# Performance work log

Measured on AMD Instinct MI355X. Metric: run time of the kernel, lower is better.

## Reference

```python
import jax, jax.numpy as jnp
import numpy as np
import math

D_MODEL = 256
N_LEVELS = 4
N_HEADS = 8
N_POINTS = 4
N_FRAME = 4
SHAPES = [(80, 80), (40, 40), (20, 20), (10, 10)]  # sum H*W = 8500
NB = 2
T1 = 4
T2 = 4
LEN_Q = 8500


def _grid_init_bias():
    # replicate torch _reset_parameters grid bias for sampling_offsets
    thetas = np.arange(N_HEADS, dtype=np.float32) * (2.0 * math.pi / N_HEADS)
    grid = np.stack([np.cos(thetas), np.sin(thetas)], -1)
    grid = grid / np.abs(grid).max(-1, keepdims=True)
    grid = np.tile(grid[:, None, None, :], (1, N_LEVELS, N_POINTS, 1))
    grid = grid * (np.arange(N_POINTS, dtype=np.float32) + 1.0)[None, None, :, None]
    return jnp.asarray(grid.reshape(-1), jnp.float32)


def setup_inputs() -> dict:
    key = jax.random.key(0)
    ks = jax.random.split(key, 8)
    Len_in = sum(h * w for h, w in SHAPES)
    query = jax.random.normal(ks[0], (NB, T1, LEN_Q, D_MODEL), jnp.float32)
    reference_points = jax.random.uniform(ks[1], (NB, T1, LEN_Q, N_LEVELS, 2), jnp.float32)
    input_flatten = jax.random.normal(ks[2], (NB, T2, Len_in, D_MODEL), jnp.float32)
    input_spatial_shapes = jnp.array(SHAPES, jnp.int32)
    starts = np.cumsum([0] + [h * w for h, w in SHAPES])[:-1]
    input_level_start_index = jnp.asarray(starts, jnp.int32)
    s = 0.01
    W_off = jax.random.normal(ks[3], (D_MODEL, N_HEADS * N_LEVELS * N_POINTS * 2), jnp.float32) * s
    b_off = _grid_init_bias()
    W_att = jax.random.normal(ks[4], (D_MODEL, N_HEADS * N_LEVELS * N_POINTS), jnp.float32) * s
    b_att = jnp.zeros((N_HEADS * N_LEVELS * N_POINTS,), jnp.float32)
    xav = 1.0 / math.sqrt(D_MODEL)
    W_val = jax.random.normal(ks[5], (D_MODEL, D_MODEL), jnp.float32) * xav
    b_val = jnp.zeros((D_MODEL,), jnp.float32)
    W_out = jax.random.normal(ks[6], (D_MODEL, D_MODEL), jnp.float32) * xav
    b_out = jnp.zeros((D_MODEL,), jnp.float32)
    return dict(query=query, reference_points=reference_points, input_flatten=input_flatten,
                input_spatial_shapes=input_spatial_shapes, input_level_start_index=input_level_start_index,
                W_off=W_off, b_off=b_off, W_att=W_att, b_att=b_att,
                W_val=W_val, b_val=b_val, W_out=W_out, b_out=b_out)


def _bilinear(v_flat, H, W, gx, gy):
    # v_flat: (B, d, H*W); gx,gy: (B, S) in [-1,1]; zeros padding, align_corners=False
    x = (gx + 1.0) * (W * 0.5) - 0.5
    y = (gy + 1.0) * (H * 0.5) - 0.5
    x0 = jnp.floor(x); y0 = jnp.floor(y)
    x1 = x0 + 1.0; y1 = y0 + 1.0
    wx1 = x - x0; wx0 = 1.0 - wx1
    wy1 = y - y0; wy0 = 1.0 - wy1

    def gather(xi, yi):
        valid = ((xi >= 0) & (xi < W) & (yi >= 0) & (yi < H)).astype(v_flat.dtype)
        xc = jnp.clip(xi, 0, W - 1).astype(jnp.int32)
        yc = jnp.clip(yi, 0, H - 1).astype(jnp.int32)
        idx = yc * W + xc  # (B, S)
        g = jnp.take_along_axis(v_flat, idx[:, None, :], axis=2)  # (B, d, S)
        return g * valid[:, None, :]

    return (gather(x0, y0) * (wx0 * wy0)[:, None, :]
            + gather(x1, y0) * (wx1 * wy0)[:, None, :]
            + gather(x0, y1) * (wx0 * wy1)[:, None, :]
            + gather(x1, y1) * (wx1 * wy1)[:, None, :])


def _core(value_t, locs, att, shapes):
    # value_t: (n, Len_in, M, d); locs: (n, Lq, M, L, P, 2); att: (n, Lq, M, L, P)
    n, Len_in, M, d = value_t.shape
    Lq, P = locs.shape[1], locs.shape[4]
    start = 0
    out = 0.0
    for l, (H, W) in enumerate(shapes):
        hw = H * W
        v = value_t[:, start:start + hw]  # (n, hw, M, d)
        start += hw
        v = v.transpose(0, 2, 3, 1).reshape(n * M, d, hw)
        g = locs[:, :, :, l] * 2.0 - 1.0  # (n, Lq, M, P, 2)
        g = g.transpose(0, 2, 1, 3, 4).reshape(n * M, Lq * P, 2)
        samp = _bilinear(v, H, W, g[..., 0], g[..., 1])  # (n*M, d, Lq*P)
        a = att[:, :, :, l].transpose(0, 2, 1, 3).reshape(n * M, 1, Lq * P)
        out = out + (samp * a).reshape(n, M, d, Lq, P).sum(-1)
    return out.transpose(0, 3, 1, 2).reshape(n, Lq, M * d)  # (n, Lq, C)


def reference(query, reference_points, input_flatten, input_spatial_shapes, input_level_start_index,
              W_off, b_off, W_att, b_att, W_val, b_val, W_out, b_out):
    shapes = [(int(h), int(w)) for h, w in np.asarray(input_spatial_shapes)]
    n, t1n, Lq, C = query.shape
    M, L, P = N_HEADS, N_LEVELS, N_POINTS
    d = C // M
    value = input_flatten @ W_val + b_val  # (n, T2, Len_in, C)
    value = value.reshape(n, value.shape[1], -1, M, d)
    normalizer = jnp.array([[w, h] for h, w in shapes], jnp.float32)  # (L, 2) = (W_l, H_l)
    outs = []
    for t1 in range(t1n):
        t2s = [t for t in (t1 - 1, t1, t1 + 1) if 0 <= t < N_FRAME]
        K = len(t2s)
        q = query[:, t1]  # (n, Lq, C)
        # all frames share ONE attention_weights Linear -> identical logits per t2
        logits = (q @ W_att + b_att).reshape(n, Lq, M, L, P)
        stacked = jnp.broadcast_to(logits[..., None], (n, Lq, M, L, P, K))
        att = jax.nn.softmax(stacked.reshape(n, Lq, M, L * P * K), axis=-1)
        att = att.reshape(n, Lq, M, L, P, K)
        # all frames share ONE sampling_offsets Linear -> identical locations per t2
        off = (q @ W_off + b_off).reshape(n, Lq, M, L, P, 2)
        off = off / normalizer[None, None, None, :, None, :]
        locs = reference_points[:, t1][:, :, None, :, None, :] + off  # (n,Lq,M,L,P,2)
        out_t1 = 0.0
        for k, t2 in enumerate(t2s):
            out_t1 = out_t1 + _core(value[:, t2], locs, att[..., k], shapes)
        outs.append(out_t1)
    out = jnp.stack(outs, axis=1)  # (n, T1, Lq, C)
    return out @ W_out + b_out
```

## Files before the change

kernel.cpp:

```cpp
#include <hip/hip_runtime.h>

#define LQ 8500

typedef _Float16 half8 __attribute__((ext_vector_type(8)));
typedef _Float16 h2 __attribute__((ext_vector_type(2)));
typedef float f32x4 __attribute__((ext_vector_type(4)));

__device__ __forceinline__ unsigned short f2h(float f) {
    return __builtin_bit_cast(unsigned short, (_Float16)f);
}
__device__ __forceinline__ float hlo(unsigned w) {
    return (float)__builtin_bit_cast(_Float16, (unsigned short)(w & 0xffffu));
}
__device__ __forceinline__ float hhi(unsigned w) {
    return (float)__builtin_bit_cast(_Float16, (unsigned short)(w >> 16));
}
__device__ __forceinline__ unsigned pk2(float a, float b) {
    return (unsigned)f2h(a) | ((unsigned)f2h(b) << 16);
}
__device__ __forceinline__ h2 toh2(unsigned w) { return __builtin_bit_cast(h2, w); }

__global__ __launch_bounds__(256) void prep_weights(const float* __restrict__ Woff,
                                                    const float* __restrict__ boff,
                                                    const float* __restrict__ Watt,
                                                    const float* __restrict__ batt,
                                                    const float* __restrict__ Wval,
                                                    const float* __restrict__ Wout,
                                                    unsigned short* __restrict__ Wct,
                                                    unsigned short* __restrict__ Wvt,
                                                    unsigned short* __restrict__ Wot,
                                                    float* __restrict__ bcat) {
    int idx = blockIdx.x * 256 + threadIdx.x;
    if (idx < 98304) {
        int j = idx >> 8, k = idx & 255;
        float v = (j < 256) ? Woff[k * 256 + j] : Watt[k * 128 + (j - 256)];
        Wct[idx] = f2h(v);
    } else if (idx < 98304 + 65536) {
        int t = idx - 98304;
        int n = t >> 8, k = t & 255;
        Wvt[t] = f2h(Wval[k * 256 + n]);
    } else if (idx < 98304 + 131072) {
        int t = idx - 98304 - 65536;
        int n = t >> 8, k = t & 255;
        Wot[t] = f2h(Wout[k * 256 + n]);
    } else if (idx < 98304 + 131072 + 384) {
        int j = idx - 98304 - 131072;
        bcat[j] = (j < 256) ? boff[j] : batt[j - 256];
    }
}

__global__ __launch_bounds__(256) void sum_frames(const float4* __restrict__ inp,
                                                  uint4* __restrict__ Xs) {
    int g = blockIdx.y;
    int t1 = g & 3, n = g >> 2;
    int f = blockIdx.x * 256 + threadIdx.x;
    if (f >= LQ * 32) return;
    int t2a = t1 == 0 ? 0 : t1 - 1;
    int t2b = t1 == 3 ? 3 : t1 + 1;
    float4 s0 = {0, 0, 0, 0}, s1 = {0, 0, 0, 0};
    for (int t2 = t2a; t2 <= t2b; ++t2) {
        const float4* p = inp + (size_t)(n * 4 + t2) * (LQ * 64) + (size_t)f * 2;
        float4 a = p[0], b = p[1];
        s0.x += a.x; s0.y += a.y; s0.z += a.z; s0.w += a.w;
        s1.x += b.x; s1.y += b.y; s1.z += b.z; s1.w += b.w;
    }
    uint4 o;
    o.x = pk2(s0.x, s0.y); o.y = pk2(s0.z, s0.w);
    o.z = pk2(s1.x, s1.y); o.w = pk2(s1.z, s1.w);
    Xs[(size_t)g * (LQ * 32) + f] = o;
}

template <int OUTMODE, int AF32>
__global__ __launch_bounds__(256) void gemm_f16(const void* __restrict__ Avoid,
                                                const unsigned short* __restrict__ Bt,
                                                const float* __restrict__ bias,
                                                void* __restrict__ Cout, int M) {
    __shared__ char lds[16384];
    const int tid = threadIdx.x;
    const int r0 = blockIdx.x * 128, c0 = blockIdx.y * 128;
    const int wid = tid >> 6, lane = tid & 63;
    const int wr = (wid >> 1) * 64, wc = (wid & 1) * 64;

    f32x4 acc[4][4] = {};

    for (int k0 = 0; k0 < 256; k0 += 32) {
#pragma unroll
        for (int cc = 0; cc < 2; ++cc) {
            int ch = cc * 256 + tid;
            int row = ch >> 2, seg = ch & 3;
            int byte = (row << 6) + (seg << 4);
            int swz = byte ^ ((row & 7) << 4);
            uint4 va = {0, 0, 0, 0};
            int ar = r0 + row;
            if (ar < M) {
                if (AF32) {
                    const float4* ap = reinterpret_cast<const float4*>(
                        (const float*)Avoid + (size_t)ar * 256 + k0 + seg * 8);
                    float4 a = ap[0], b = ap[1];
                    va.x = pk2(a.x, a.y); va.y = pk2(a.z, a.w);
                    va.z = pk2(b.x, b.y); va.w = pk2(b.z, b.w);
                } else {
                    va = *reinterpret_cast<const uint4*>(
                        (const unsigned short*)Avoid + (size_t)ar * 256 + k0 + seg * 8);
                }
            }
            *reinterpret_cast<uint4*>(lds + swz) = va;
            uint4 vb = *reinterpret_cast<const uint4*>(Bt + (size_t)(c0 + row) * 256 + k0 + seg * 8);
            *reinterpret_cast<uint4*>(lds + 8192 + swz) = vb;
        }
        __syncthreads();
        half8 af[4], bf[4];
#pragma unroll
        for (int i = 0; i < 4; ++i) {
            int rowA = wr + i * 16 + (lane & 15);
            int byteA = (rowA << 6) + ((lane >> 4) << 4);
            af[i] = *reinterpret_cast<const half8*>(lds + (byteA ^ ((rowA & 7) << 4)));
            int rowB = wc + i * 16 + (lane & 15);
            int byteB = (rowB << 6) + ((lane >> 4) << 4);
            bf[i] = *reinterpret_cast<const half8*>(lds + 8192 + (byteB ^ ((rowB & 7) << 4)));
        }
#pragma unroll
        for (int i = 0; i < 4; ++i)
#pragma unroll
            for (int j = 0; j < 4; ++j)
                acc[i][j] = __builtin_amdgcn_mfma_f32_16x16x32_f16(af[i], bf[j], acc[i][j], 0, 0, 0);
        __syncthreads();
    }

#pragma unroll
    for (int j = 0; j < 4; ++j) {
        int col = c0 + wc + j * 16 + (lane & 15);
        float bv = bias[col];
#pragma unroll
        for (int i = 0; i < 4; ++i) {
#pragma unroll
            for (int r = 0; r < 4; ++r) {
                int row = r0 + wr + i * 16 + (lane >> 4) * 4 + r;
                if (row >= M) continue;
                float v = acc[i][j][r];
                if (OUTMODE == 1) {
                    int g = row / LQ;
                    int pos = row - g * LQ;
                    int t1 = g & 3;
                    float sc = (t1 == 0 || t1 == 3) ? 2.f : 3.f;
                    v += bv * sc;
                    int m = col >> 5, c = col & 31;
                    ((unsigned short*)Cout)[((size_t)(g * 8 + m) * LQ + pos) * 32 + c] = f2h(v);
                } else if (OUTMODE == 2) {
                    ((unsigned short*)Cout)[(size_t)row * 384 + col] = f2h(v + bv);
                } else {
                    ((float*)Cout)[(size_t)row * 256 + col] = v + bv;
                }
            }
        }
    }
}

__global__ __launch_bounds__(256) void sample_kernel(const unsigned short* __restrict__ P,
                                                     const float* __restrict__ refp,
                                                     const unsigned short* __restrict__ Vs,
                                                     unsigned short* __restrict__ O16) {
    int tid = threadIdx.x, bid = blockIdx.x;
    int g = bid & 7;
    int q0 = (bid >> 3) * 16;
    int ql = tid >> 4, m = (tid >> 1) & 7, h = tid & 1;
    int q = q0 + ql;
    if (q >= LQ) return;

    const size_t qrow = (size_t)g * LQ + q;

    unsigned ow[16];
    {
        const uint4* po = reinterpret_cast<const uint4*>(P + qrow * 384 + m * 32);
        uint4 a = po[0], b = po[1], c = po[2], d = po[3];
        ow[0] = a.x; ow[1] = a.y; ow[2] = a.z; ow[3] = a.w;
        ow[4] = b.x; ow[5] = b.y; ow[6] = b.z; ow[7] = b.w;
        ow[8] = c.x; ow[9] = c.y; ow[10] = c.z; ow[11] = c.w;
        ow[12] = d.x; ow[13] = d.y; ow[14] = d.z; ow[15] = d.w;
    }
    float wgt[16];
    {
        const uint4* pa = reinterpret_cast<const uint4*>(P + qrow * 384 + 256 + m * 16);
        uint4 a = pa[0], b = pa[1];
        unsigned aw[8] = {a.x, a.y, a.z, a.w, b.x, b.y, b.z, b.w};
#pragma unroll
        for (int j = 0; j < 8; ++j) {
            wgt[j * 2 + 0] = hlo(aw[j]);
            wgt[j * 2 + 1] = hhi(aw[j]);
        }
        float mx = -1e30f;
#pragma unroll
        for (int j = 0; j < 16; ++j) mx = fmaxf(mx, wgt[j]);
        float s = 0.f;
#pragma unroll
        for (int j = 0; j < 16; ++j) { wgt[j] = __expf(wgt[j] - mx); s += wgt[j]; }
        int t1 = g & 3;
        float Kc = (t1 == 0 || t1 == 3) ? 2.f : 3.f;
        float inv = 1.f / (s * Kc);
#pragma unroll
        for (int j = 0; j < 16; ++j) wgt[j] *= inv;
    }

    float rx[4], ry[4];
    {
        const float4* rp = reinterpret_cast<const float4*>(refp + qrow * 8);
        float4 r0 = rp[0], r1 = rp[1];
        rx[0] = r0.x; ry[0] = r0.y; rx[1] = r0.z; ry[1] = r0.w;
        rx[2] = r1.x; ry[2] = r1.y; rx[3] = r1.z; ry[3] = r1.w;
    }

    h2 acc[8];
#pragma unroll
    for (int d = 0; d < 8; ++d) acc[d] = h2{(_Float16)0.f, (_Float16)0.f};

    const unsigned short* vplane = Vs + (size_t)(g * 8 + m) * (LQ * 32) + h * 16;

#pragma unroll
    for (int p = 0; p < 16; ++p) {
        const int l = p >> 2;
        const int Wl = 80 >> l;
        const int start = (l == 0) ? 0 : (l == 1) ? 6400 : (l == 2) ? 8000 : 8400;
        const float Wlf = (float)Wl;

        float x = fmaf(rx[l], Wlf, hlo(ow[p])) - 0.5f;
        float y = fmaf(ry[l], Wlf, hhi(ow[p])) - 0.5f;
        float w = wgt[p];

        float xf = floorf(x), yf = floorf(y);
        int x0 = (int)xf, y0 = (int)yf;
        float wx1 = x - xf, wy1 = y - yf;

        int xb = min(max(x0, 0), Wl - 2);
        float wl = (x0 == xb) ? 1.f - wx1 : ((x0 + 1 == xb) ? wx1 : 0.f);
        float wr = (x0 == xb) ? wx1 : ((x0 - 1 == xb) ? 1.f - wx1 : 0.f);

        int yc[2];
        float cw[2];
        yc[0] = min(max(y0, 0), Wl - 1);
        cw[0] = (y0 >= 0 && y0 < Wl) ? (1.f - wy1) * w : 0.f;
        int y1i = y0 + 1;
        yc[1] = min(max(y1i, 0), Wl - 1);
        cw[1] = (y1i >= 0 && y1i < Wl) ? wy1 * w : 0.f;

#pragma unroll
        for (int ryi = 0; ryi < 2; ++ryi) {
            float clf = cw[ryi] * wl, crf = cw[ryi] * wr;
            _Float16 clh = (_Float16)clf, crh = (_Float16)crf;
            h2 cl2 = {clh, clh}, cr2 = {crh, crh};
            const uint4* vp = reinterpret_cast<const uint4*>(
                vplane + (size_t)(start + yc[ryi] * Wl + xb) * 32);
            uint4 La = vp[0], Lb = vp[1];
            uint4 Ra = vp[4], Rb = vp[5];
            acc[0] += cl2 * toh2(La.x) + cr2 * toh2(Ra.x);
            acc[1] += cl2 * toh2(La.y) + cr2 * toh2(Ra.y);
            acc[2] += cl2 * toh2(La.z) + cr2 * toh2(Ra.z);
            acc[3] += cl2 * toh2(La.w) + cr2 * toh2(Ra.w);
            acc[4] += cl2 * toh2(Lb.x) + cr2 * toh2(Rb.x);
            acc[5] += cl2 * toh2(Lb.y) + cr2 * toh2(Rb.y);
            acc[6] += cl2 * toh2(Lb.z) + cr2 * toh2(Rb.z);
            acc[7] += cl2 * toh2(Lb.w) + cr2 * toh2(Rb.w);
        }
    }

    unsigned short* op = O16 + qrow * 256 + m * 32 + h * 16;
    uint4 o0, o1;
    o0.x = __builtin_bit_cast(unsigned, acc[0]);
    o0.y = __builtin_bit_cast(unsigned, acc[1]);
    o0.z = __builtin_bit_cast(unsigned, acc[2]);
    o0.w = __builtin_bit_cast(unsigned, acc[3]);
    o1.x = __builtin_bit_cast(unsigned, acc[4]);
    o1.y = __builtin_bit_cast(unsigned, acc[5]);
    o1.z = __builtin_bit_cast(unsigned, acc[6]);
    o1.w = __builtin_bit_cast(unsigned, acc[7]);
    reinterpret_cast<uint4*>(op)[0] = o0;
    reinterpret_cast<uint4*>(op)[1] = o1;
}

extern "C" void kernel_launch(void* const* d_in, const int* in_sizes, int n_in,
                              void* d_out, int out_size, void* d_ws, size_t ws_size,
                              hipStream_t stream) {
    const float* query = (const float*)d_in[0];
    const float* refp  = (const float*)d_in[1];
    const float* inp   = (const float*)d_in[2];
    const float* Woff = (const float*)d_in[5];
    const float* boff = (const float*)d_in[6];
    const float* Watt = (const float*)d_in[7];
    const float* batt = (const float*)d_in[8];
    const float* Wval = (const float*)d_in[9];
    const float* bval = (const float*)d_in[10];
    const float* Wout = (const float*)d_in[11];
    const float* bout = (const float*)d_in[12];
    float* out = (float*)d_out;

    char* base = (char*)d_ws;
    unsigned short* Xs16 = (unsigned short*)base;
    unsigned short* Vs   = (unsigned short*)(base + 34816000);
    unsigned short* P    = (unsigned short*)(base + 69632000);
    unsigned short* Wct  = (unsigned short*)(base + 121856000);
    unsigned short* Wvt  = (unsigned short*)(base + 122052608);
    unsigned short* Wot  = (unsigned short*)(base + 122183680);
    float* bcat          = (float*)(base + 122314752);
    unsigned short* O16  = Xs16;

    prep_weights<<<dim3(898), 256, 0, stream>>>(Woff, boff, Watt, batt, Wval, Wout,
                                                Wct, Wvt, Wot, bcat);

    sum_frames<<<dim3((LQ * 32 + 255) / 256, 8), 256, 0, stream>>>(
        (const float4*)inp, (uint4*)Xs16);

    gemm_f16<1, 0><<<dim3((8 * LQ + 127) / 128, 2), 256, 0, stream>>>(
        Xs16, Wvt, bval, Vs, 8 * LQ);

    gemm_f16<2, 1><<<dim3((8 * LQ + 127) / 128, 3), 256, 0, stream>>>(
        query, Wct, bcat, P, 8 * LQ);

    sample_kernel<<<dim3(((LQ + 15) / 16) * 8), 256, 0, stream>>>(P, refp, Vs, O16);

    gemm_f16<0, 0><<<dim3((8 * LQ + 127) / 128, 2), 256, 0, stream>>>(
        O16, Wot, bout, out, 8 * LQ);
}
```

Before: 363.7 us.

## Fuse frame summation into value GEMM, stage full-K A tile in LDS

Measured after the change: 435.9 us. +19.9%, slower.

```diff
diff --git a/kernel.cpp b/kernel.cpp
--- a/kernel.cpp
+++ b/kernel.cpp
@@ -19,6 +19,10 @@
     return (unsigned)f2h(a) | ((unsigned)f2h(b) << 16);
 }
 __device__ __forceinline__ h2 toh2(unsigned w) { return __builtin_bit_cast(h2, w); }
+__device__ __forceinline__ h2 bc2(float f) {
+    _Float16 h = (_Float16)f;
+    return h2{h, h};
+}
 
 __global__ __launch_bounds__(256) void prep_weights(const float* __restrict__ Woff,
                                                     const float* __restrict__ boff,
@@ -49,82 +53,94 @@
     }
 }
 
-__global__ __launch_bounds__(256) void sum_frames(const float4* __restrict__ inp,
-                                                  uint4* __restrict__ Xs) {
-    int g = blockIdx.y;
-    int t1 = g & 3, n = g >> 2;
-    int f = blockIdx.x * 256 + threadIdx.x;
-    if (f >= LQ * 32) return;
-    int t2a = t1 == 0 ? 0 : t1 - 1;
-    int t2b = t1 == 3 ? 3 : t1 + 1;
-    float4 s0 = {0, 0, 0, 0}, s1 = {0, 0, 0, 0};
-    for (int t2 = t2a; t2 <= t2b; ++t2) {
-        const float4* p = inp + (size_t)(n * 4 + t2) * (LQ * 64) + (size_t)f * 2;
-        float4 a = p[0], b = p[1];
-        s0.x += a.x; s0.y += a.y; s0.z += a.z; s0.w += a.w;
-        s1.x += b.x; s1.y += b.y; s1.z += b.z; s1.w += b.w;
-    }
-    uint4 o;
-    o.x = pk2(s0.x, s0.y); o.y = pk2(s0.z, s0.w);
-    o.z = pk2(s1.x, s1.y); o.w = pk2(s1.z, s1.w);
-    Xs[(size_t)g * (LQ * 32) + f] = o;
-}
-
-template <int OUTMODE, int AF32>
+template <int OUTMODE, int ASRC>
 __global__ __launch_bounds__(256) void gemm_f16(const void* __restrict__ Avoid,
                                                 const unsigned short* __restrict__ Bt,
                                                 const float* __restrict__ bias,
                                                 void* __restrict__ Cout, int M) {
-    __shared__ char lds[16384];
+    __shared__ char lds[65536];
     const int tid = threadIdx.x;
-    const int r0 = blockIdx.x * 128, c0 = blockIdx.y * 128;
+    const int c0 = blockIdx.x * 128, r0 = blockIdx.y * 128;
     const int wid = tid >> 6, lane = tid & 63;
     const int wr = (wid >> 1) * 64, wc = (wid & 1) * 64;
 
+#pragma unroll
+    for (int i = 0; i < 16; ++i) {
+        int c = i * 256 + tid;
+        int t = c >> 9;
+        int row = (c >> 2) & 127;
+        int seg = c & 3;
+        int koff = t * 32 + seg * 8;
+        int ar = r0 + row;
+        uint4 va = {0, 0, 0, 0};
+        if (ar < M) {
+            if (ASRC == 0) {
+                va = *reinterpret_cast<const uint4*>(
+                    (const unsigned short*)Avoid + (size_t)ar * 256 + koff);
+            } else if (ASRC == 1) {
+                const float4* ap = reinterpret_cast<const float4*>(
+                    (const float*)Avoid + (size_t)ar * 256 + koff);
+                float4 a = ap[0], b = ap[1];
+                va.x = pk2(a.x, a.y); va.y = pk2(a.z, a.w);
+                va.z = pk2(b.x, b.y); va.w = pk2(b.z, b.w);
+            } else {
+                int g = ar / LQ;
+                int pos = ar - g * LQ;
+                int t1 = g & 3, n = g >> 2;
+                int tp = t1 == 0 ? 0 : t1 - 1;
+                int tn = t1 == 3 ? 3 : t1 + 1;
+                const float* fb = (const float*)Avoid;
+                const float4* pm = reinterpret_cast<const float4*>(
+                    fb + ((size_t)(n * 4 + t1) * LQ + pos) * 256 + koff);
+                const float4* pp = reinterpret_cast<const float4*>(
+                    fb + ((size_t)(n * 4 + tp) * LQ + pos) * 256 + koff);
+                const float4* pn = reinterpret_cast<const float4*>(
+                    fb + ((size_t)(n * 4 + tn) * LQ + pos) * 256 + koff);
+                float4 m0 = pm[0], m1 = pm[1];
+                float4 a0 = pp[0], a1 = pp[1];
+                float4 b0 = pn[0], b1 = pn[1];
+                float fp = (t1 > 0) ? 1.f : 0.f;
+                float fn = (t1 < 3) ? 1.f : 0.f;
+                float4 s0, s1;
+                s0.x = m0.x + fp * a0.x + fn * b0.x;
+                s0.y = m0.y + fp * a0.y + fn * b0.y;
+                s0.z = m0.z + fp * a0.z + fn * b0.z;
+                s0.w = m0.w + fp * a0.w + fn * b0.w;
+                s1.x = m1.x + fp * a1.x + fn * b1.x;
+                s1.y = m1.y + fp * a1.y + fn * b1.y;
+                s1.z = m1.z + fp * a1.z + fn * b1.z;
+                s1.w = m1.w + fp * a1.w + fn * b1.w;
+                va.x = pk2(s0.x, s0.y); va.y = pk2(s0.z, s0.w);
+                va.z = pk2(s1.x, s1.y); va.w = pk2(s1.z, s1.w);
+            }
+        }
+        int byte = (row << 6) + (seg << 4);
+        int swz = byte ^ ((row & 7) << 4);
+        *reinterpret_cast<uint4*>(lds + t * 8192 + swz) = va;
+    }
+    __syncthreads();
+
     f32x4 acc[4][4] = {};
-
-    for (int k0 = 0; k0 < 256; k0 += 32) {
-#pragma unroll
-        for (int cc = 0; cc < 2; ++cc) {
-            int ch = cc * 256 + tid;
-            int row = ch >> 2, seg = ch & 3;
-            int byte = (row << 6) + (seg << 4);
-            int swz = byte ^ ((row & 7) << 4);
-            uint4 va = {0, 0, 0, 0};
-            int ar = r0 + row;
-            if (ar < M) {
-                if (AF32) {
-                    const float4* ap = reinterpret_cast<const float4*>(
-                        (const float*)Avoid + (size_t)ar * 256 + k0 + seg * 8);
-                    float4 a = ap[0], b = ap[1];
-                    va.x = pk2(a.x, a.y); va.y = pk2(a.z, a.w);
-                    va.z = pk2(b.x, b.y); va.w = pk2(b.z, b.w);
-                } else {
-                    va = *reinterpret_cast<const uint4*>(
-                        (const unsigned short*)Avoid + (size_t)ar * 256 + k0 + seg * 8);
-                }
-            }
-            *reinterpret_cast<uint4*>(lds + swz) = va;
-            uint4 vb = *reinterpret_cast<const uint4*>(Bt + (size_t)(c0 + row) * 256 + k0 + seg * 8);
-            *reinterpret_cast<uint4*>(lds + 8192 + swz) = vb;
-        }
-        __syncthreads();
+    for (int t = 0; t < 8; ++t) {
+        char* base = lds + t * 8192;
         half8 af[4], bf[4];
+#pragma unroll
+        for (int j = 0; j < 4; ++j) {
+            int rowB = c0 + wc + j * 16 + (lane & 15);
+            bf[j] = *reinterpret_cast<const half8*>(
+                Bt + (size_t)rowB * 256 + t * 32 + (lane >> 4) * 8);
+        }
 #pragma unroll
         for (int i = 0; i < 4; ++i) {
             int rowA = wr + i * 16 + (lane & 15);
             int byteA = (rowA << 6) + ((lane >> 4) << 4);
-            af[i] = *reinterpret_cast<const half8*>(lds + (byteA ^ ((rowA & 7) << 4)));
-            int rowB = wc + i * 16 + (lane & 15);
-            int byteB = (rowB << 6) + ((lane >> 4) << 4);
-            bf[i] = *reinterpret_cast<const half8*>(lds + 8192 + (byteB ^ ((rowB & 7) << 4)));
+            af[i] = *reinterpret_cast<const half8*>(base + (byteA ^ ((rowA & 7) << 4)));
         }
 #pragma unroll
         for (int i = 0; i < 4; ++i)
 #pragma unroll
             for (int j = 0; j < 4; ++j)
                 acc[i][j] = __builtin_amdgcn_mfma_f32_16x16x32_f16(af[i], bf[j], acc[i][j], 0, 0, 0);
-        __syncthreads();
     }
 
 #pragma unroll
@@ -215,7 +231,7 @@
 
     const unsigned short* vplane = Vs + (size_t)(g * 8 + m) * (LQ * 32) + h * 16;
 
-#pragma unroll
+#pragma unroll 4
     for (int p = 0; p < 16; ++p) {
         const int l = p >> 2;
         const int Wl = 80 >> l;
@@ -234,32 +250,30 @@
         float wl = (x0 == xb) ? 1.f - wx1 : ((x0 + 1 == xb) ? wx1 : 0.f);
         float wr = (x0 == xb) ? wx1 : ((x0 - 1 == xb) ? 1.f - wx1 : 0.f);
 
-        int yc[2];
-        float cw[2];
-        yc[0] = min(max(y0, 0), Wl - 1);
-        cw[0] = (y0 >= 0 && y0 < Wl) ? (1.f - wy1) * w : 0.f;
+        int yc0 = min(max(y0, 0), Wl - 1);
+        float cw0 = (y0 >= 0 && y0 < Wl) ? (1.f - wy1) * w : 0.f;
         int y1i = y0 + 1;
-        yc[1] = min(max(y1i, 0), Wl - 1);
-        cw[1] = (y1i >= 0 && y1i < Wl) ? wy1 * w : 0.f;
-
-#pragma unroll
-        for (int ryi = 0; ryi < 2; ++ryi) {
-            float clf = cw[ryi] * wl, crf = cw[ryi] * wr;
-            _Float16 clh = (_Float16)clf, crh = (_Float16)crf;
-            h2 cl2 = {clh, clh}, cr2 = {crh, crh};
-            const uint4* vp = reinterpret_cast<const uint4*>(
-                vplane + (size_t)(start + yc[ryi] * Wl + xb) * 32);
-            uint4 La = vp[0], Lb = vp[1];
-            uint4 Ra = vp[4], Rb = vp[5];
-            acc[0] += cl2 * toh2(La.x) + cr2 * toh2(Ra.x);
-            acc[1] += cl2 * toh2(La.y) + cr2 * toh2(Ra.y);
-            acc[2] += cl2 * toh2(La.z) + cr2 * toh2(Ra.z);
-            acc[3] += cl2 * toh2(La.w) + cr2 * toh2(Ra.w);
-            acc[4] += cl2 * toh2(Lb.x) + cr2 * toh2(Rb.x);
-            acc[5] += cl2 * toh2(Lb.y) + cr2 * toh2(Rb.y);
-            acc[6] += cl2 * toh2(Lb.z) + cr2 * toh2(Rb.z);
-            acc[7] += cl2 * toh2(Lb.w) + cr2 * toh2(Rb.w);
-        }
+        int yc1 = min(max(y1i, 0), Wl - 1);
+        float cw1 = (y1i >= 0 && y1i < Wl) ? wy1 * w : 0.f;
+
+        const uint4* p0 = reinterpret_cast<const uint4*>(
+            vplane + (size_t)(start + yc0 * Wl + xb) * 32);
+        const uint4* p1 = reinterpret_cast<const uint4*>(
+            vplane + (size_t)(start + yc1 * Wl + xb) * 32);
+        uint4 L0a = p0[0], L0b = p0[1], R0a = p0[4], R0b = p0[5];
+        uint4 L1a = p1[0], L1b = p1[1], R1a = p1[4], R1b = p1[5];
+
+        h2 c0l = bc2(cw0 * wl), c0r = bc2(cw0 * wr);
+        h2 c1l = bc2(cw1 * wl), c1r = bc2(cw1 * wr);
+
+        acc[0] += c0l * toh2(L0a.x) + c0r * toh2(R0a.x) + c1l * toh2(L1a.x) + c1r * toh2(R1a.x);
+        acc[1] += c0l * toh2(L0a.y) + c0r * toh2(R0a.y) + c1l * toh2(L1a.y) + c1r * toh2(R1a.y);
+        acc[2] += c0l * toh2(L0a.z) + c0r * toh2(R0a.z) + c1l * toh2(L1a.z) + c1r * toh2(R1a.z);
+        acc[3] += c0l * toh2(L0a.w) + c0r * toh2(R0a.w) + c1l * toh2(L1a.w) + c1r * toh2(R1a.w);
+        acc[4] += c0l * toh2(L0b.x) + c0r * toh2(R0b.x) + c1l * toh2(L1b.x) + c1r * toh2(R1b.x);
+        acc[5] += c0l * toh2(L0b.y) + c0r * toh2(R0b.y) + c1l * toh2(L1b.y) + c1r * toh2(R1b.y);
+        acc[6] += c0l * toh2(L0b.z) + c0r * toh2(R0b.z) + c1l * toh2(L1b.z) + c1r * toh2(R1b.z);
+        acc[7] += c0l * toh2(L0b.w) + c0r * toh2(R0b.w) + c1l * toh2(L1b.w) + c1r * toh2(R1b.w);
     }
 
     unsigned short* op = O16 + qrow * 256 + m * 32 + h * 16;
@@ -293,29 +307,24 @@
     float* out = (float*)d_out;
 
     char* base = (char*)d_ws;
-    unsigned short* Xs16 = (unsigned short*)base;
-    unsigned short* Vs   = (unsigned short*)(base + 34816000);
-    unsigned short* P    = (unsigned short*)(base + 69632000);
+    unsigned short* Vs   = (unsigned short*)base;
+    unsigned short* P    = (unsigned short*)(base + 34816000);
+    unsigned short* O16  = (unsigned short*)(base + 87040000);
     unsigned short* Wct  = (unsigned short*)(base + 121856000);
     unsigned short* Wvt  = (unsigned short*)(base + 122052608);
     unsigned short* Wot  = (unsigned short*)(base + 122183680);
     float* bcat          = (float*)(base + 122314752);
-    unsigned short* O16  = Xs16;
+
+    const int RT = (8 * LQ + 127) / 128;
 
     prep_weights<<<dim3(898), 256, 0, stream>>>(Woff, boff, Watt, batt, Wval, Wout,
                                                 Wct, Wvt, Wot, bcat);
 
-    sum_frames<<<dim3((LQ * 32 + 255) / 256, 8), 256, 0, stream>>>(
-        (const float4*)inp, (uint4*)Xs16);
-
-    gemm_f16<1, 0><<<dim3((8 * LQ + 127) / 128, 2), 256, 0, stream>>>(
-        Xs16, Wvt, bval, Vs, 8 * LQ);
-
-    gemm_f16<2, 1><<<dim3((8 * LQ + 127) / 128, 3), 256, 0, stream>>>(
-        query, Wct, bcat, P, 8 * LQ);
+    gemm_f16<1, 2><<<dim3(2, RT), 256, 0, stream>>>(inp, Wvt, bval, Vs, 8 * LQ);
+
+    gemm_f16<2, 1><<<dim3(3, RT), 256, 0, stream>>>(query, Wct, bcat, P, 8 * LQ);
 
     sample_kernel<<<dim3(((LQ + 15) / 16) * 8), 256, 0, stream>>>(P, refp, Vs, O16);
 
-    gemm_f16<0, 0><<<dim3((8 * LQ + 127) / 128, 2), 256, 0, stream>>>(
-        O16, Wot, bout, out, 8 * LQ);
-}
+    gemm_f16<0, 0><<<dim3(2, RT), 256, 0, stream>>>(O16, Wot, bout, out, 8 * LQ);
+}
```
